# Optimization experiments

Hardware: AMD Instinct MI355X
Metric: run time of the kernel (lower is better)

## Reference

```python
import jax, jax.numpy as jnp
import numpy as np

N1, N2, G_DIM, R_DIM, NF = 4000, 4000, 8000, 20000, 3
M1, M2, MG, MR = 1200, 1200, 2400, 6000
ALPHA = (1000.0, 1000.0, 100.0, 0.0)


def setup_inputs() -> dict:
    key = jax.random.key(0)
    ks = jax.random.split(key, 16)
    return {
        "G": jax.random.uniform(ks[0], (N1, G_DIM), dtype=jnp.float32),
        "R": jax.random.uniform(ks[1], (N2, R_DIM), dtype=jnp.float32),
        "A": jax.random.uniform(ks[2], (G_DIM, R_DIM), dtype=jnp.float32),
        "C_1": jax.random.uniform(ks[3], (N1, NF), dtype=jnp.float32),
        "C_2": jax.random.uniform(ks[4], (N2, NF), dtype=jnp.float32),
        "C_g": jax.random.uniform(ks[5], (G_DIM, NF), dtype=jnp.float32),
        "C_r": jax.random.uniform(ks[6], (R_DIM, NF), dtype=jnp.float32),
        "Ai": jax.random.normal(ks[7], (NF, NF), dtype=jnp.float32),
        "b_g": jnp.zeros((1, G_DIM), dtype=jnp.float32),
        "b_r": jnp.zeros((1, R_DIM), dtype=jnp.float32),
        "b_1": jnp.zeros((N1, 1), dtype=jnp.float32),
        "b_2": jnp.zeros((N2, 1), dtype=jnp.float32),
        "mask_1": jax.random.randint(ks[8], (M1,), 0, N1, dtype=jnp.int32),
        "mask_2": jax.random.randint(ks[9], (M2,), 0, N2, dtype=jnp.int32),
        "mask_g": jax.random.randint(ks[10], (MG,), 0, G_DIM, dtype=jnp.int32),
        "mask_r": jax.random.randint(ks[11], (MR,), 0, R_DIM, dtype=jnp.int32),
    }


def _sm(X):
    # softmax over factor dim (dim=1)
    return jax.nn.softmax(X, axis=1)


def _entropy_loss(C):
    return -jnp.mean((_sm(C) - 0.5) ** 2)


def reference(G, R, A, C_1, C_2, C_g, C_r, Ai, b_g, b_r, b_1, b_2,
              mask_1, mask_2, mask_g, mask_r):
    sg = jax.lax.stop_gradient
    # --- mode == 'C_gr' branch of batch_loss ---
    # masked gathers (np.ix_ style: rows then cols)
    G_sub = G[mask_1][:, mask_g]                      # [M1, MG]
    R_sub = R[mask_2][:, mask_r]                      # [M2, MR]
    A_sub = A[mask_g][:, mask_r]                      # [MG, MR]

    P1 = _sm(sg(C_1[mask_1]))                         # [M1, N] (detached)
    P2 = _sm(sg(C_2[mask_2]))                         # [M2, N] (detached)
    Pg = _sm(C_g[mask_g])                             # [MG, N]
    Pr = _sm(C_r[mask_r])                             # [MR, N]
    Ai_d = sg(Ai)

    pred_G = (P1 @ Ai_d) @ Pg.T                       # [M1, MG], tiny-rank matmul
    loss1 = jnp.mean((G_sub - pred_G - b_g[:, mask_g] - b_1[mask_1]) ** 2)

    pred_R = (P2 @ Ai_d) @ Pr.T                       # [M2, MR]
    loss2 = jnp.mean((R_sub - pred_R - b_r[:, mask_r] - b_2[mask_2]) ** 2)

    # trace alignment: -tr((Pg/|Pg|)^T A_sub (Pr/|Pr|)) = -sum((A_sub @ Prn) * Pgn)
    Pgn = Pg / jnp.linalg.norm(Pg)
    Prn = Pr / jnp.linalg.norm(Pr)
    loss3 = -jnp.sum((A_sub @ Prn) * Pgn)

    loss4 = (_entropy_loss(sg(C_1[mask_1])) + _entropy_loss(sg(C_2[mask_2]))
             + _entropy_loss(C_g[mask_g]) + _entropy_loss(C_r[mask_r]))

    loss = ALPHA[0] * loss1 + ALPHA[1] * loss2 + ALPHA[2] * loss3 + ALPHA[3] * loss4
    return jnp.stack([loss, ALPHA[0] * loss1, ALPHA[1] * loss2,
                      ALPHA[2] * loss3, ALPHA[3] * loss4])
```

## Files before the change

### kernel.cpp

```cpp
#include <hip/hip_runtime.h>
#include <math.h>

#define N1v    4000
#define N2v    4000
#define G_DIMv 8000
#define R_DIMv 20000
#define M1v    1200
#define M2v    1200
#define MGv    2400
#define MRv    6000

#define ACC_N 8

#define CH   60
#define JB1  10
#define JB23 24
#define IC1  20
#define IC2  20
#define IC3  40
#define S1_BLOCKS (JB1*IC1)
#define S2_BLOCKS (JB23*IC2)
#define S3_BLOCKS (JB23*IC3)
#define TOTAL_BLOCKS (S1_BLOCKS + S2_BLOCKS + S3_BLOCKS)

__device__ __forceinline__ void softmax3(float a, float b, float c,
                                         float& p0, float& p1, float& p2) {
    float m = fmaxf(a, fmaxf(b, c));
    float e0 = expf(a - m), e1 = expf(b - m), e2 = expf(c - m);
    float inv = 1.0f / (e0 + e1 + e2);
    p0 = e0 * inv; p1 = e1 * inv; p2 = e2 * inv;
}

__global__ void norm_kernel(const float* __restrict__ Cg, const float* __restrict__ Cr,
                            const int* __restrict__ mg, const int* __restrict__ mr,
                            float* __restrict__ ws) {
    int idx = blockIdx.x * 256 + threadIdx.x;
    float vg = 0.0f, vr = 0.0f;
    if (idx < MGv) {
        int r = mg[idx];
        float p0, p1, p2;
        softmax3(Cg[r*3], Cg[r*3+1], Cg[r*3+2], p0, p1, p2);
        vg = p0*p0 + p1*p1 + p2*p2;
    } else if (idx < MGv + MRv) {
        int i = idx - MGv;
        int r = mr[i];
        float p0, p1, p2;
        softmax3(Cr[r*3], Cr[r*3+1], Cr[r*3+2], p0, p1, p2);
        vr = p0*p0 + p1*p1 + p2*p2;
    }
    #pragma unroll
    for (int o = 32; o > 0; o >>= 1) {
        vg += __shfl_down(vg, o, 64);
        vr += __shfl_down(vr, o, 64);
    }
    __shared__ float sA[4], sB[4];
    int lane = threadIdx.x & 63, w = threadIdx.x >> 6;
    if (lane == 0) { sA[w] = vg; sB[w] = vr; }
    __syncthreads();
    if (threadIdx.x == 0) {
        atomicAdd(&ws[3], sA[0] + sA[1] + sA[2] + sA[3]);
        atomicAdd(&ws[4], sB[0] + sB[1] + sB[2] + sB[3]);
    }
}

__global__ __launch_bounds__(256) void main_kernel(
    const float* __restrict__ G, const float* __restrict__ R, const float* __restrict__ A,
    const float* __restrict__ C1, const float* __restrict__ C2,
    const float* __restrict__ Cg, const float* __restrict__ Cr,
    const float* __restrict__ Ai,
    const float* __restrict__ bg, const float* __restrict__ br,
    const float* __restrict__ b1, const float* __restrict__ b2,
    const int* __restrict__ m1, const int* __restrict__ m2,
    const int* __restrict__ mg, const int* __restrict__ mr,
    float* __restrict__ ws) {
    __shared__ int   s_row[CH];
    __shared__ float s_vec[CH * 3];
    __shared__ float s_bias[CH];
    __shared__ float s_red[4];

    int bid = blockIdx.x;
    int sec, jb, chunk;
    if (bid < S1_BLOCKS)                  { sec = 0; jb = bid % JB1;  chunk = bid / JB1; }
    else if (bid < S1_BLOCKS + S2_BLOCKS) { int b = bid - S1_BLOCKS;  sec = 1; jb = b % JB23; chunk = b / JB23; }
    else                                  { int b = bid - S1_BLOCKS - S2_BLOCKS; sec = 2; jb = b % JB23; chunk = b / JB23; }

    const int *rmask, *cmask;
    const float *rsrc, *csrc, *data, *biasr, *biasc;
    int NIs, NJs; long stride;
    if (sec == 0) {
        rmask = m1; cmask = mg; rsrc = C1; csrc = Cg; data = G;
        biasr = b1; biasc = bg; NIs = M1v; NJs = MGv; stride = G_DIMv;
    } else if (sec == 1) {
        rmask = m2; cmask = mr; rsrc = C2; csrc = Cr; data = R;
        biasr = b2; biasc = br; NIs = M2v; NJs = MRv; stride = R_DIMv;
    } else {
        rmask = mg; cmask = mr; rsrc = Cg; csrc = Cr; data = A;
        biasr = nullptr; biasc = nullptr; NIs = MGv; NJs = MRv; stride = R_DIMv;
    }

    int tid = threadIdx.x;
    int j = jb * 256 + tid;
    bool jvalid = j < NJs;

    int cj = 0; float v0 = 0, v1 = 0, v2 = 0, bc = 0;
    if (jvalid) {
        cj = cmask[j];
        softmax3(csrc[cj*3], csrc[cj*3+1], csrc[cj*3+2], v0, v1, v2);
        if (biasc) bc = biasc[cj];
    }

    int i0 = chunk * CH;
    for (int t = tid; t < CH; t += 256) {
        int ii = i0 + t;
        if (ii < NIs) {
            int r = rmask[ii];
            float p0, p1, p2;
            softmax3(rsrc[r*3], rsrc[r*3+1], rsrc[r*3+2], p0, p1, p2);
            float w0, w1, w2;
            if (sec == 2) { w0 = p0; w1 = p1; w2 = p2; }
            else {
                w0 = p0*Ai[0] + p1*Ai[3] + p2*Ai[6];
                w1 = p0*Ai[1] + p1*Ai[4] + p2*Ai[7];
                w2 = p0*Ai[2] + p1*Ai[5] + p2*Ai[8];
            }
            s_row[t] = r;
            s_vec[t*3]   = w0;
            s_vec[t*3+1] = w1;
            s_vec[t*3+2] = w2;
            s_bias[t] = biasr ? biasr[r] : 0.0f;
        } else {
            s_row[t] = 0;
            s_vec[t*3] = s_vec[t*3+1] = s_vec[t*3+2] = 0.0f;
            s_bias[t] = 0.0f;
        }
    }
    __syncthreads();

    float acc = 0.0f;
    int nmax = NIs - i0; if (nmax > CH) nmax = CH;
    if (jvalid) {
        if (sec == 2) {
            for (int t = 0; t < nmax; t++) {
                long row = s_row[t];
                float x = data[row * stride + cj];
                float dot = s_vec[t*3]*v0 + s_vec[t*3+1]*v1 + s_vec[t*3+2]*v2;
                acc += x * dot;
            }
        } else {
            for (int t = 0; t < nmax; t++) {
                long row = s_row[t];
                float x = data[row * stride + cj];
                float pred = s_vec[t*3]*v0 + s_vec[t*3+1]*v1 + s_vec[t*3+2]*v2;
                float d = x - pred - bc - s_bias[t];
                acc += d * d;
            }
        }
    }

    #pragma unroll
    for (int o = 32; o > 0; o >>= 1) acc += __shfl_down(acc, o, 64);
    int lane = tid & 63, w = tid >> 6;
    if (lane == 0) s_red[w] = acc;
    __syncthreads();
    if (tid == 0) {
        float tot = s_red[0] + s_red[1] + s_red[2] + s_red[3];
        atomicAdd(&ws[sec], tot);
    }
}

__global__ void finalize_kernel(const float* __restrict__ ws, float* __restrict__ out) {
    if (threadIdx.x == 0 && blockIdx.x == 0) {
        float l1 = ws[0] * (1.0f / (float)(M1v * MGv)) * 1000.0f;
        float l2 = ws[1] * (1.0f / (float)(M2v * MRv)) * 1000.0f;
        float l3 = -ws[2] / sqrtf(ws[3] * ws[4]) * 100.0f;
        out[0] = l1 + l2 + l3;
        out[1] = l1;
        out[2] = l2;
        out[3] = l3;
        out[4] = 0.0f;
    }
}

extern "C" void kernel_launch(void* const* d_in, const int* in_sizes, int n_in,
                              void* d_out, int out_size, void* d_ws, size_t ws_size,
                              hipStream_t stream) {
    const float* G  = (const float*)d_in[0];
    const float* R  = (const float*)d_in[1];
    const float* A  = (const float*)d_in[2];
    const float* C1 = (const float*)d_in[3];
    const float* C2 = (const float*)d_in[4];
    const float* Cg = (const float*)d_in[5];
    const float* Cr = (const float*)d_in[6];
    const float* Ai = (const float*)d_in[7];
    const float* bg = (const float*)d_in[8];
    const float* br = (const float*)d_in[9];
    const float* b1 = (const float*)d_in[10];
    const float* b2 = (const float*)d_in[11];
    const int* m1 = (const int*)d_in[12];
    const int* m2 = (const int*)d_in[13];
    const int* mg = (const int*)d_in[14];
    const int* mr = (const int*)d_in[15];
    float* ws  = (float*)d_ws;
    float* out = (float*)d_out;

    hipMemsetAsync(d_ws, 0, ACC_N * sizeof(float), stream);
    norm_kernel<<<(MGv + MRv + 255) / 256, 256, 0, stream>>>(Cg, Cr, mg, mr, ws);
    main_kernel<<<TOTAL_BLOCKS, 256, 0, stream>>>(G, R, A, C1, C2, Cg, Cr, Ai,
                                                  bg, br, b1, b2, m1, m2, mg, mr, ws);
    finalize_kernel<<<1, 64, 0, stream>>>(ws, out);
}
```

Before: 1.098 ms.

## Replace masked gathers with histogram-weighted dense row/column sweeps

Builds per-index multiplicity histograms for each mask and compacts the unique selected rows. Each loss is then computed over unique rows and all columns, with columns weighted by sqrt(count) or count, so the duplicate-aware sum matches the gathered version. This swaps scattered scalar column gathers for contiguous float4 row loads, at the cost of reading every column of each selected row and adding extra preprocessing kernels plus a larger workspace memset. Float summation order changes, so results may differ slightly.

```diff
diff --git a/kernel.cpp b/kernel.cpp
--- a/kernel.cpp
+++ b/kernel.cpp
@@ -1,27 +1,47 @@
 #include <hip/hip_runtime.h>
 #include <math.h>
 
-#define N1v    4000
-#define N2v    4000
-#define G_DIMv 8000
-#define R_DIMv 20000
-#define M1v    1200
-#define M2v    1200
-#define MGv    2400
-#define MRv    6000
-
-#define ACC_N 8
-
-#define CH   60
-#define JB1  10
-#define JB23 24
-#define IC1  20
-#define IC2  20
-#define IC3  40
-#define S1_BLOCKS (JB1*IC1)
-#define S2_BLOCKS (JB23*IC2)
-#define S3_BLOCKS (JB23*IC3)
-#define TOTAL_BLOCKS (S1_BLOCKS + S2_BLOCKS + S3_BLOCKS)
+#define N1v 4000
+#define N2v 4000
+#define GDv 8000
+#define RDv 20000
+#define M1v 1200
+#define M2v 1200
+#define MGv 2400
+#define MRv 6000
+
+#define W_ACC    0
+#define W_NC     8
+#define W_CNT1   16
+#define W_CNT2   (W_CNT1 + N1v)
+#define W_CNTG   (W_CNT2 + N2v)
+#define W_CNTR   (W_CNTG + GDv)
+#define W_ZEND   (W_CNTR + RDv)
+#define W_COLG4  W_ZEND
+#define W_COLGB  (W_COLG4 + 4*GDv)
+#define W_COLR24 (W_COLGB + GDv)
+#define W_COLR2B (W_COLR24 + 4*RDv)
+#define W_COLR34 (W_COLR2B + RDv)
+#define W_R1ID   (W_COLR34 + 4*RDv)
+#define W_R14    (W_R1ID + M1v)
+#define W_R1C    (W_R14 + 4*M1v)
+#define W_R2ID   (W_R1C + M1v)
+#define W_R24    (W_R2ID + M2v)
+#define W_R2C    (W_R24 + 4*M2v)
+#define W_R3ID   (W_R2C + M2v)
+#define W_R34    (W_R3ID + MGv)
+#define W_R3C    (W_R34 + 4*MGv)
+
+#define RC  32
+#define CT  2048
+#define T1  4
+#define T23 10
+#define CH12 38
+#define CH3  75
+#define S1B (T1*CH12)
+#define S2B (T23*CH12)
+#define S3B (T23*CH3)
+#define TOTB (S1B + S2B + S3B)
 
 __device__ __forceinline__ void softmax3(float a, float b, float c,
                                          float& p0, float& p1, float& p2) {
@@ -31,22 +51,46 @@
     p0 = e0 * inv; p1 = e1 * inv; p2 = e2 * inv;
 }
 
-__global__ void norm_kernel(const float* __restrict__ Cg, const float* __restrict__ Cr,
+__global__ void hist_kernel(const int* __restrict__ m1, const int* __restrict__ m2,
                             const int* __restrict__ mg, const int* __restrict__ mr,
                             float* __restrict__ ws) {
     int idx = blockIdx.x * 256 + threadIdx.x;
+    int* cnt1 = (int*)(ws + W_CNT1);
+    int* cnt2 = (int*)(ws + W_CNT2);
+    int* cntg = (int*)(ws + W_CNTG);
+    int* cntr = (int*)(ws + W_CNTR);
+    if (idx < M1v)                          atomicAdd(&cnt1[m1[idx]], 1);
+    else if (idx < M1v + M2v)               atomicAdd(&cnt2[m2[idx - M1v]], 1);
+    else if (idx < M1v + M2v + MGv)         atomicAdd(&cntg[mg[idx - M1v - M2v]], 1);
+    else if (idx < M1v + M2v + MGv + MRv)   atomicAdd(&cntr[mr[idx - M1v - M2v - MGv]], 1);
+}
+
+__global__ void colstate_kernel(const float* __restrict__ Cg, const float* __restrict__ Cr,
+                                const float* __restrict__ bg, const float* __restrict__ br,
+                                float* __restrict__ ws) {
+    int idx = blockIdx.x * 256 + threadIdx.x;
+    const int* cntg = (const int*)(ws + W_CNTG);
+    const int* cntr = (const int*)(ws + W_CNTR);
     float vg = 0.0f, vr = 0.0f;
-    if (idx < MGv) {
-        int r = mg[idx];
+    if (idx < GDv) {
+        int c = idx;
+        float n = (float)cntg[c];
         float p0, p1, p2;
-        softmax3(Cg[r*3], Cg[r*3+1], Cg[r*3+2], p0, p1, p2);
-        vg = p0*p0 + p1*p1 + p2*p2;
-    } else if (idx < MGv + MRv) {
-        int i = idx - MGv;
-        int r = mr[i];
+        softmax3(Cg[c*3], Cg[c*3+1], Cg[c*3+2], p0, p1, p2);
+        float s = sqrtf(n);
+        ((float4*)(ws + W_COLG4))[c] = make_float4(s*p0, s*p1, s*p2, s);
+        ws[W_COLGB + c] = s * bg[c];
+        vg = n * (p0*p0 + p1*p1 + p2*p2);
+    } else if (idx < GDv + RDv) {
+        int c = idx - GDv;
+        float n = (float)cntr[c];
         float p0, p1, p2;
-        softmax3(Cr[r*3], Cr[r*3+1], Cr[r*3+2], p0, p1, p2);
-        vr = p0*p0 + p1*p1 + p2*p2;
+        softmax3(Cr[c*3], Cr[c*3+1], Cr[c*3+2], p0, p1, p2);
+        float s = sqrtf(n);
+        ((float4*)(ws + W_COLR24))[c] = make_float4(s*p0, s*p1, s*p2, s);
+        ws[W_COLR2B + c] = s * br[c];
+        ((float4*)(ws + W_COLR34))[c] = make_float4(n*p0, n*p1, n*p2, 0.0f);
+        vr = n * (p0*p0 + p1*p1 + p2*p2);
     }
     #pragma unroll
     for (int o = 32; o > 0; o >>= 1) {
@@ -63,98 +107,152 @@
     }
 }
 
+__global__ void rowcompact_kernel(const float* __restrict__ C1, const float* __restrict__ C2,
+                                  const float* __restrict__ Cg, const float* __restrict__ Ai,
+                                  const float* __restrict__ b1, const float* __restrict__ b2,
+                                  float* __restrict__ ws) {
+    int idx = blockIdx.x * 256 + threadIdx.x;
+    int* nc = (int*)(ws + W_NC);
+    if (idx < N1v) {
+        int r = idx;
+        int c = ((const int*)(ws + W_CNT1))[r];
+        if (c > 0) {
+            int k = atomicAdd(&nc[0], 1);
+            float p0, p1, p2;
+            softmax3(C1[r*3], C1[r*3+1], C1[r*3+2], p0, p1, p2);
+            float w0 = p0*Ai[0] + p1*Ai[3] + p2*Ai[6];
+            float w1 = p0*Ai[1] + p1*Ai[4] + p2*Ai[7];
+            float w2 = p0*Ai[2] + p1*Ai[5] + p2*Ai[8];
+            ((int*)(ws + W_R1ID))[k] = r;
+            ((float4*)(ws + W_R14))[k] = make_float4(w0, w1, w2, b1[r]);
+            ws[W_R1C + k] = (float)c;
+        }
+    } else if (idx < N1v + N2v) {
+        int r = idx - N1v;
+        int c = ((const int*)(ws + W_CNT2))[r];
+        if (c > 0) {
+            int k = atomicAdd(&nc[1], 1);
+            float p0, p1, p2;
+            softmax3(C2[r*3], C2[r*3+1], C2[r*3+2], p0, p1, p2);
+            float w0 = p0*Ai[0] + p1*Ai[3] + p2*Ai[6];
+            float w1 = p0*Ai[1] + p1*Ai[4] + p2*Ai[7];
+            float w2 = p0*Ai[2] + p1*Ai[5] + p2*Ai[8];
+            ((int*)(ws + W_R2ID))[k] = r;
+            ((float4*)(ws + W_R24))[k] = make_float4(w0, w1, w2, b2[r]);
+            ws[W_R2C + k] = (float)c;
+        }
+    } else if (idx < N1v + N2v + GDv) {
+        int g = idx - N1v - N2v;
+        int c = ((const int*)(ws + W_CNTG))[g];
+        if (c > 0) {
+            int k = atomicAdd(&nc[2], 1);
+            float p0, p1, p2;
+            softmax3(Cg[g*3], Cg[g*3+1], Cg[g*3+2], p0, p1, p2);
+            ((int*)(ws + W_R3ID))[k] = g;
+            ((float4*)(ws + W_R34))[k] = make_float4(p0, p1, p2, 0.0f);
+            ws[W_R3C + k] = (float)c;
+        }
+    }
+}
+
 __global__ __launch_bounds__(256) void main_kernel(
     const float* __restrict__ G, const float* __restrict__ R, const float* __restrict__ A,
-    const float* __restrict__ C1, const float* __restrict__ C2,
-    const float* __restrict__ Cg, const float* __restrict__ Cr,
-    const float* __restrict__ Ai,
-    const float* __restrict__ bg, const float* __restrict__ br,
-    const float* __restrict__ b1, const float* __restrict__ b2,
-    const int* __restrict__ m1, const int* __restrict__ m2,
-    const int* __restrict__ mg, const int* __restrict__ mr,
     float* __restrict__ ws) {
-    __shared__ int   s_row[CH];
-    __shared__ float s_vec[CH * 3];
-    __shared__ float s_bias[CH];
+    int bid = blockIdx.x;
+    int sec, tile, chunk;
+    if (bid < S1B)            { sec = 0; tile = bid / CH12; chunk = bid % CH12; }
+    else if (bid < S1B + S2B) { int b = bid - S1B; sec = 1; tile = b / CH12; chunk = b % CH12; }
+    else                      { int b = bid - S1B - S2B; sec = 2; tile = b / CH3; chunk = b % CH3; }
+
+    const float *data; const float4 *cst; const float *cbias;
+    const int *rid; const float4 *rst; const float *rcn;
+    int NC; long stride; int nidx;
+    if (sec == 0) {
+        data = G; stride = GDv; NC = GDv;
+        cst = (const float4*)(ws + W_COLG4); cbias = ws + W_COLGB;
+        rid = (const int*)(ws + W_R1ID); rst = (const float4*)(ws + W_R14); rcn = ws + W_R1C;
+        nidx = 0;
+    } else if (sec == 1) {
+        data = R; stride = RDv; NC = RDv;
+        cst = (const float4*)(ws + W_COLR24); cbias = ws + W_COLR2B;
+        rid = (const int*)(ws + W_R2ID); rst = (const float4*)(ws + W_R24); rcn = ws + W_R2C;
+        nidx = 1;
+    } else {
+        data = A; stride = RDv; NC = RDv;
+        cst = (const float4*)(ws + W_COLR34); cbias = nullptr;
+        rid = (const int*)(ws + W_R3ID); rst = (const float4*)(ws + W_R34); rcn = ws + W_R3C;
+        nidx = 2;
+    }
+
+    int n = ((const int*)(ws + W_NC))[nidx];
+    int r0 = chunk * RC;
+    if (r0 >= n) return;
+    int nr = min(n - r0, RC);
+
+    __shared__ int   s_rid[RC];
+    __shared__ float4 s_rw[RC];
+    __shared__ float s_rc[RC];
     __shared__ float s_red[4];
-
-    int bid = blockIdx.x;
-    int sec, jb, chunk;
-    if (bid < S1_BLOCKS)                  { sec = 0; jb = bid % JB1;  chunk = bid / JB1; }
-    else if (bid < S1_BLOCKS + S2_BLOCKS) { int b = bid - S1_BLOCKS;  sec = 1; jb = b % JB23; chunk = b / JB23; }
-    else                                  { int b = bid - S1_BLOCKS - S2_BLOCKS; sec = 2; jb = b % JB23; chunk = b / JB23; }
-
-    const int *rmask, *cmask;
-    const float *rsrc, *csrc, *data, *biasr, *biasc;
-    int NIs, NJs; long stride;
-    if (sec == 0) {
-        rmask = m1; cmask = mg; rsrc = C1; csrc = Cg; data = G;
-        biasr = b1; biasc = bg; NIs = M1v; NJs = MGv; stride = G_DIMv;
-    } else if (sec == 1) {
-        rmask = m2; cmask = mr; rsrc = C2; csrc = Cr; data = R;
-        biasr = b2; biasc = br; NIs = M2v; NJs = MRv; stride = R_DIMv;
-    } else {
-        rmask = mg; cmask = mr; rsrc = Cg; csrc = Cr; data = A;
-        biasr = nullptr; biasc = nullptr; NIs = MGv; NJs = MRv; stride = R_DIMv;
-    }
-
     int tid = threadIdx.x;
-    int j = jb * 256 + tid;
-    bool jvalid = j < NJs;
-
-    int cj = 0; float v0 = 0, v1 = 0, v2 = 0, bc = 0;
-    if (jvalid) {
-        cj = cmask[j];
-        softmax3(csrc[cj*3], csrc[cj*3+1], csrc[cj*3+2], v0, v1, v2);
-        if (biasc) bc = biasc[cj];
-    }
-
-    int i0 = chunk * CH;
-    for (int t = tid; t < CH; t += 256) {
-        int ii = i0 + t;
-        if (ii < NIs) {
-            int r = rmask[ii];
-            float p0, p1, p2;
-            softmax3(rsrc[r*3], rsrc[r*3+1], rsrc[r*3+2], p0, p1, p2);
-            float w0, w1, w2;
-            if (sec == 2) { w0 = p0; w1 = p1; w2 = p2; }
-            else {
-                w0 = p0*Ai[0] + p1*Ai[3] + p2*Ai[6];
-                w1 = p0*Ai[1] + p1*Ai[4] + p2*Ai[7];
-                w2 = p0*Ai[2] + p1*Ai[5] + p2*Ai[8];
-            }
-            s_row[t] = r;
-            s_vec[t*3]   = w0;
-            s_vec[t*3+1] = w1;
-            s_vec[t*3+2] = w2;
-            s_bias[t] = biasr ? biasr[r] : 0.0f;
-        } else {
-            s_row[t] = 0;
-            s_vec[t*3] = s_vec[t*3+1] = s_vec[t*3+2] = 0.0f;
-            s_bias[t] = 0.0f;
-        }
+    if (tid < RC && tid < nr) {
+        s_rid[tid] = rid[r0 + tid];
+        s_rw[tid]  = rst[r0 + tid];
+        s_rc[tid]  = rcn[r0 + tid];
     }
     __syncthreads();
 
+    int cc0 = tile * CT + 4 * tid;
+    int cc1 = cc0 + 1024;
+    bool v0 = (cc0 < NC);
+    bool v1 = (cc1 < NC);
+
+    float4 ca[8];
+    float  cb[8];
+    #pragma unroll
+    for (int q = 0; q < 8; q++) { ca[q] = make_float4(0,0,0,0); cb[q] = 0.0f; }
+    if (v0) {
+        #pragma unroll
+        for (int q = 0; q < 4; q++) ca[q] = cst[cc0 + q];
+        if (sec < 2) {
+            #pragma unroll
+            for (int q = 0; q < 4; q++) cb[q] = cbias[cc0 + q];
+        }
+    }
+    if (v1) {
+        #pragma unroll
+        for (int q = 0; q < 4; q++) ca[4+q] = cst[cc1 + q];
+        if (sec < 2) {
+            #pragma unroll
+            for (int q = 0; q < 4; q++) cb[4+q] = cbias[cc1 + q];
+        }
+    }
+
     float acc = 0.0f;
-    int nmax = NIs - i0; if (nmax > CH) nmax = CH;
-    if (jvalid) {
-        if (sec == 2) {
-            for (int t = 0; t < nmax; t++) {
-                long row = s_row[t];
-                float x = data[row * stride + cj];
-                float dot = s_vec[t*3]*v0 + s_vec[t*3+1]*v1 + s_vec[t*3+2]*v2;
-                acc += x * dot;
+    for (int ir = 0; ir < nr; ir++) {
+        long rrow = s_rid[ir];
+        float4 rw = s_rw[ir];
+        float  rc = s_rc[ir];
+        const float* drow = data + rrow * stride;
+        float4 x0 = v0 ? *(const float4*)(drow + cc0) : make_float4(0,0,0,0);
+        float4 x1 = v1 ? *(const float4*)(drow + cc1) : make_float4(0,0,0,0);
+        float xs[8] = {x0.x, x0.y, x0.z, x0.w, x1.x, x1.y, x1.z, x1.w};
+        float racc = 0.0f;
+        if (sec < 2) {
+            #pragma unroll
+            for (int q = 0; q < 8; q++) {
+                float rp = ca[q].w * (xs[q] - rw.w)
+                         - (rw.x*ca[q].x + rw.y*ca[q].y + rw.z*ca[q].z)
+                         - cb[q];
+                racc = fmaf(rp, rp, racc);
             }
         } else {
-            for (int t = 0; t < nmax; t++) {
-                long row = s_row[t];
-                float x = data[row * stride + cj];
-                float pred = s_vec[t*3]*v0 + s_vec[t*3+1]*v1 + s_vec[t*3+2]*v2;
-                float d = x - pred - bc - s_bias[t];
-                acc += d * d;
+            #pragma unroll
+            for (int q = 0; q < 8; q++) {
+                float d = rw.x*ca[q].x + rw.y*ca[q].y + rw.z*ca[q].z;
+                racc = fmaf(xs[q], d, racc);
             }
         }
+        acc = fmaf(rc, racc, acc);
     }
 
     #pragma unroll
@@ -162,10 +260,7 @@
     int lane = tid & 63, w = tid >> 6;
     if (lane == 0) s_red[w] = acc;
     __syncthreads();
-    if (tid == 0) {
-        float tot = s_red[0] + s_red[1] + s_red[2] + s_red[3];
-        atomicAdd(&ws[sec], tot);
-    }
+    if (tid == 0) atomicAdd(&ws[nidx], s_red[0] + s_red[1] + s_red[2] + s_red[3]);
 }
 
 __global__ void finalize_kernel(const float* __restrict__ ws, float* __restrict__ out) {
@@ -203,9 +298,10 @@
     float* ws  = (float*)d_ws;
     float* out = (float*)d_out;
 
-    hipMemsetAsync(d_ws, 0, ACC_N * sizeof(float), stream);
-    norm_kernel<<<(MGv + MRv + 255) / 256, 256, 0, stream>>>(Cg, Cr, mg, mr, ws);
-    main_kernel<<<TOTAL_BLOCKS, 256, 0, stream>>>(G, R, A, C1, C2, Cg, Cr, Ai,
-                                                  bg, br, b1, b2, m1, m2, mg, mr, ws);
+    hipMemsetAsync(d_ws, 0, (size_t)W_ZEND * 4, stream);
+    hist_kernel<<<(M1v + M2v + MGv + MRv + 255) / 256, 256, 0, stream>>>(m1, m2, mg, mr, ws);
+    colstate_kernel<<<(GDv + RDv + 255) / 256, 256, 0, stream>>>(Cg, Cr, bg, br, ws);
+    rowcompact_kernel<<<(N1v + N2v + GDv + 255) / 256, 256, 0, stream>>>(C1, C2, Cg, Ai, b1, b2, ws);
+    main_kernel<<<TOTB, 256, 0, stream>>>(G, R, A, ws);
     finalize_kernel<<<1, 64, 0, stream>>>(ws, out);
 }
```

Result: faster. 948.3 us (-13.6%).
